# Performance work log

Measured on AMD Instinct MI355X. Metric: run time of the kernel, lower is better.

The kernel has to match this reference:

```python
import jax, jax.numpy as jnp
import numpy as np

N_NODES = 100000
N_EDGES = 1600000
N_GRAPHS = 64
IN_F = 128
H_F = 128
N_CLS = 10


def setup_inputs() -> dict:
    key = jax.random.key(0)
    ks = jax.random.split(key, 10)
    feat = jax.random.normal(ks[0], (N_NODES, IN_F), dtype=jnp.float32)
    W1 = jax.random.normal(ks[1], (IN_F, H_F), dtype=jnp.float32) * 0.05
    b1 = jax.random.normal(ks[2], (H_F,), dtype=jnp.float32) * 0.05
    W2 = jax.random.normal(ks[3], (H_F, H_F), dtype=jnp.float32) * 0.05
    b2 = jax.random.normal(ks[4], (H_F,), dtype=jnp.float32) * 0.05
    Wp = jax.random.normal(ks[5], (H_F, N_CLS), dtype=jnp.float32) * 0.05
    bp = jax.random.normal(ks[6], (N_CLS,), dtype=jnp.float32) * 0.05
    src = jax.random.randint(ks[7], (N_EDGES,), 0, N_NODES, dtype=jnp.int32)
    dst = jax.random.randint(ks[8], (N_EDGES,), 0, N_NODES, dtype=jnp.int32)
    graph_id = jnp.sort(jax.random.randint(ks[9], (N_NODES,), 0, N_GRAPHS, dtype=jnp.int32))
    return {"feat": feat, "W1": W1, "b1": b1, "W2": W2, "b2": b2,
            "Wp": Wp, "bp": bp, "src": src, "dst": dst, "graph_id": graph_id}


def reference(feat, W1, b1, W2, b2, Wp, bp, src, dst, graph_id):
    # copy_u + sum: each dst node sums features of its source neighbors
    def agg(h):
        return jax.ops.segment_sum(h[src], dst, num_segments=N_NODES)

    h = jax.nn.relu(agg(feat) @ W1 + b1)   # conv1 + ReLU
    h = jax.nn.relu(agg(h) @ W2 + b2)      # conv2 + ReLU (num_messagepasses=2)

    # dgl.mean_nodes: per-graph mean pooling over nodes
    sums = jax.ops.segment_sum(h, graph_id, num_segments=N_GRAPHS)      # [G, H]
    cnts = jax.ops.segment_sum(jnp.ones((N_NODES, 1), h.dtype), graph_id,
                               num_segments=N_GRAPHS)                    # [G, 1]
    graph_feats = sums / jnp.maximum(cnts, 1.0)
    return graph_feats @ Wp + bp
```

## Files before the change

### kernel.cpp

```cpp
#include <hip/hip_runtime.h>

#define NF 128
#define NGRAPHS 64
#define NCLS 10
#define NPARTS 256
#define PART_SHIFT 9
#define PART_NODES 512
#define PART_CAP 9216
#define SPLIT_TILE 4096
#define AS_STRIDE 136
#define SRC_BITS 17

typedef __attribute__((ext_vector_type(8))) short bf16x8;
typedef __attribute__((ext_vector_type(4))) float f32x4;
typedef __attribute__((ext_vector_type(8))) unsigned short u16x8;

__device__ __forceinline__ float bf2f(unsigned short u) {
    union { unsigned int i; float f; } v; v.i = ((unsigned int)u) << 16; return v.f;
}
__device__ __forceinline__ unsigned short f2bf(float f) {
    union { float f; unsigned int i; } v; v.f = f;
    unsigned int lsb = (v.i >> 16) & 1;
    v.i += 0x7fffu + lsb;
    return (unsigned short)(v.i >> 16);
}

__device__ __forceinline__ void gather_node(
    const unsigned short* __restrict__ x, const int* __restrict__ offs,
    const int* __restrict__ eid, int node, int n, int c, float acc[8]) {
#pragma unroll
    for (int r = 0; r < 8; ++r) acc[r] = 0.f;
    if (node >= n) return;
    int j = offs[node];
    int end = offs[node + 1];
    for (; j + 8 <= end; j += 8) {
        int s0 = eid[j + 0], s1 = eid[j + 1], s2 = eid[j + 2], s3 = eid[j + 3];
        int s4 = eid[j + 4], s5 = eid[j + 5], s6 = eid[j + 6], s7 = eid[j + 7];
        u16x8 v0 = ((const u16x8*)(x + (size_t)s0 * NF))[c];
        u16x8 v1 = ((const u16x8*)(x + (size_t)s1 * NF))[c];
        u16x8 v2 = ((const u16x8*)(x + (size_t)s2 * NF))[c];
        u16x8 v3 = ((const u16x8*)(x + (size_t)s3 * NF))[c];
        u16x8 v4 = ((const u16x8*)(x + (size_t)s4 * NF))[c];
        u16x8 v5 = ((const u16x8*)(x + (size_t)s5 * NF))[c];
        u16x8 v6 = ((const u16x8*)(x + (size_t)s6 * NF))[c];
        u16x8 v7 = ((const u16x8*)(x + (size_t)s7 * NF))[c];
#pragma unroll
        for (int r = 0; r < 8; ++r)
            acc[r] += ((bf2f(v0[r]) + bf2f(v1[r])) + (bf2f(v2[r]) + bf2f(v3[r])))
                    + ((bf2f(v4[r]) + bf2f(v5[r])) + (bf2f(v6[r]) + bf2f(v7[r])));
    }
    if (j + 4 <= end) {
        int s0 = eid[j + 0], s1 = eid[j + 1], s2 = eid[j + 2], s3 = eid[j + 3];
        u16x8 v0 = ((const u16x8*)(x + (size_t)s0 * NF))[c];
        u16x8 v1 = ((const u16x8*)(x + (size_t)s1 * NF))[c];
        u16x8 v2 = ((const u16x8*)(x + (size_t)s2 * NF))[c];
        u16x8 v3 = ((const u16x8*)(x + (size_t)s3 * NF))[c];
#pragma unroll
        for (int r = 0; r < 8; ++r)
            acc[r] += (bf2f(v0[r]) + bf2f(v1[r])) + (bf2f(v2[r]) + bf2f(v3[r]));
        j += 4;
    }
    for (; j < end; ++j) {
        int s0 = eid[j];
        u16x8 v0 = ((const u16x8*)(x + (size_t)s0 * NF))[c];
#pragma unroll
        for (int r = 0; r < 8; ++r) acc[r] += bf2f(v0[r]);
    }
}

__global__ __launch_bounds__(256) void split_prep_kernel(
    const int* __restrict__ src, const int* __restrict__ dst,
    unsigned int* __restrict__ records, int* __restrict__ gcur,
    const float* __restrict__ feat, unsigned short* __restrict__ featbf,
    const float* __restrict__ W1, const float* __restrict__ W2,
    unsigned short* __restrict__ Wt1, unsigned short* __restrict__ Wt2,
    float* __restrict__ sums, int ne, int nv4) {
    __shared__ unsigned int stage[SPLIT_TILE];
    __shared__ int hcnt[NPARTS];
    __shared__ int hscan[NPARTS];
    __shared__ int hcur[NPARTS];
    __shared__ int hg[NPARTS];
    int t = threadIdx.x;
    int gtid = blockIdx.x * 256 + t;
    int nthreads = gridDim.x * 256;

    for (int i = gtid; i < nv4; i += nthreads) {
        float4 v = ((const float4*)feat)[i];
        ushort4 o;
        o.x = f2bf(v.x); o.y = f2bf(v.y); o.z = f2bf(v.z); o.w = f2bf(v.w);
        ((ushort4*)featbf)[i] = o;
    }
    for (int i = gtid; i < 2 * NF * NF; i += nthreads) {
        const float* W = (i < NF * NF) ? W1 : W2;
        unsigned short* Wt = (i < NF * NF) ? Wt1 : Wt2;
        int id = i & (NF * NF - 1);
        int f = id >> 7;
        int k = id & 127;
        Wt[f * NF + k] = f2bf(W[k * NF + f]);
    }
    for (int i = gtid; i < NGRAPHS * NF; i += nthreads) sums[i] = 0.f;

    int tile0 = blockIdx.x * SPLIT_TILE;
    int cnt = min(SPLIT_TILE, ne - tile0);
    if (cnt <= 0) return;
    hcnt[t] = 0;
    __syncthreads();
    int dv[16], sv[16];
#pragma unroll
    for (int k2 = 0; k2 < 16; ++k2) {
        int i = k2 * 256 + t;
        if (i < cnt) {
            dv[k2] = dst[tile0 + i];
            sv[k2] = src[tile0 + i];
            atomicAdd(&hcnt[dv[k2] >> PART_SHIFT], 1);
        }
    }
    __syncthreads();
    hscan[t] = hcnt[t];
    __syncthreads();
    for (int off = 1; off < NPARTS; off <<= 1) {
        int v = (t >= off) ? hscan[t - off] : 0;
        __syncthreads();
        hscan[t] += v;
        __syncthreads();
    }
    hcur[t] = hscan[t] - hcnt[t];
    hg[t] = hcnt[t] ? atomicAdd(&gcur[t], hcnt[t]) : 0;
    __syncthreads();
#pragma unroll
    for (int k2 = 0; k2 < 16; ++k2) {
        int i = k2 * 256 + t;
        if (i < cnt) {
            int d = dv[k2];
            int pos = atomicAdd(&hcur[d >> PART_SHIFT], 1);
            stage[pos] = (((unsigned int)(d & (PART_NODES - 1))) << SRC_BITS)
                         | (unsigned int)sv[k2];
        }
    }
    __syncthreads();
    int grp = t >> 4;
    int lt = t & 15;
    for (int p = grp; p < NPARTS; p += 16) {
        int c = hcnt[p];
        if (c == 0) continue;
        int b = hscan[p] - c;
        int g = hg[p];
        if (g + c > PART_CAP) c = max(0, PART_CAP - g);
        unsigned int* outp = records + (size_t)p * PART_CAP + g;
        for (int i = lt; i < c; i += 16) outp[i] = stage[b + i];
    }
}

__global__ __launch_bounds__(256) void build_kernel(
    const unsigned int* __restrict__ records, const int* __restrict__ gcur,
    int* __restrict__ offs, int* __restrict__ eid, int n) {
    __shared__ int deg[PART_NODES];
    __shared__ int ps[NPARTS];
    __shared__ int wsum[4];
    __shared__ unsigned int rc[PART_CAP];
    int t = threadIdx.x;
    int p = blockIdx.x;

    ps[t] = min(gcur[t], PART_CAP);
    __syncthreads();
    for (int off = 1; off < NPARTS; off <<= 1) {
        int v = (t >= off) ? ps[t - off] : 0;
        __syncthreads();
        ps[t] += v;
        __syncthreads();
    }
    int L = min(gcur[p], PART_CAP);
    int base_g = ps[p] - L;
    if (p == 0 && t == 0) offs[n] = ps[NPARTS - 1];

    int lo = p << PART_SHIFT;
    int nn = min(n - lo, PART_NODES);
    if (nn <= 0) return;

    deg[t] = 0;
    deg[t + 256] = 0;
    __syncthreads();

    const unsigned int* rp = records + (size_t)p * PART_CAP;
    for (int i = t; i < L; i += 256) {
        unsigned int r = rp[i];
        rc[i] = r;
        atomicAdd(&deg[r >> SRC_BITS], 1);
    }
    __syncthreads();

    int v0 = deg[2 * t];
    int v1 = deg[2 * t + 1];
    int tsum = v0 + v1;
    int lane = t & 63, w = t >> 6;
    int sc = tsum;
    for (int off = 1; off < 64; off <<= 1) {
        int u = __shfl_up(sc, off, 64);
        if (lane >= off) sc += u;
    }
    if (lane == 63) wsum[w] = sc;
    __syncthreads();
    if (t == 0) {
        int a = 0;
        for (int k = 0; k < 4; ++k) { int v = wsum[k]; wsum[k] = a; a += v; }
    }
    __syncthreads();
    int run = sc - tsum + wsum[w];
    deg[2 * t] = run;
    if (2 * t < nn) offs[lo + 2 * t] = base_g + run;
    run += v0;
    deg[2 * t + 1] = run;
    if (2 * t + 1 < nn) offs[lo + 2 * t + 1] = base_g + run;
    __syncthreads();

    for (int i = t; i < L; i += 256) {
        unsigned int r = rc[i];
        int pos = atomicAdd(&deg[r >> SRC_BITS], 1);
        eid[base_g + pos] = (int)(r & ((1u << SRC_BITS) - 1));
    }
}

__global__ __launch_bounds__(256) void gather_gemm1(
    const unsigned short* __restrict__ x, const int* __restrict__ offs,
    const int* __restrict__ eid, const unsigned short* __restrict__ Wt,
    const float* __restrict__ bias, unsigned short* __restrict__ out, int n) {
    __shared__ unsigned short As[16 * AS_STRIDE];
    int wave = threadIdx.x >> 6;
    int lane = threadIdx.x & 63;
    int q = lane >> 4;
    int c = lane & 15;
    int node_base = blockIdx.x * 16;
    int row = wave * 4 + q;

    float acc[8];
    gather_node(x, offs, eid, node_base + row, n, c, acc);
    {
        u16x8 o;
#pragma unroll
        for (int r = 0; r < 8; ++r) o[r] = f2bf(acc[r]);
        *(u16x8*)(&As[row * AS_STRIDE + c * 8]) = o;
    }
    __syncthreads();

    int m16 = c;
    int n0 = wave * 32;
    const unsigned short* b0r = Wt + (size_t)(n0 + m16) * NF + q * 8;
    const unsigned short* b1r = b0r + 16 * NF;
    f32x4 acc0 = {0.f, 0.f, 0.f, 0.f};
    f32x4 acc1 = {0.f, 0.f, 0.f, 0.f};
#pragma unroll
    for (int kk = 0; kk < 4; ++kk) {
        bf16x8 a  = *(const bf16x8*)(&As[m16 * AS_STRIDE + kk * 32 + q * 8]);
        bf16x8 b0 = *(const bf16x8*)(b0r + kk * 32);
        bf16x8 b1 = *(const bf16x8*)(b1r + kk * 32);
        acc0 = __builtin_amdgcn_mfma_f32_16x16x32_bf16(a, b0, acc0, 0, 0, 0);
        acc1 = __builtin_amdgcn_mfma_f32_16x16x32_bf16(a, b1, acc1, 0, 0, 0);
    }
    float bias0 = bias[n0 + m16];
    float bias1 = bias[n0 + 16 + m16];
#pragma unroll
    for (int r = 0; r < 4; ++r) {
        int node = node_base + q * 4 + r;
        if (node >= n) break;
        unsigned short* o = out + (size_t)node * NF;
        o[n0 + m16]      = f2bf(fmaxf(acc0[r] + bias0, 0.f));
        o[n0 + 16 + m16] = f2bf(fmaxf(acc1[r] + bias1, 0.f));
    }
}

__global__ __launch_bounds__(256) void gather_gemm2_pool(
    const unsigned short* __restrict__ x, const int* __restrict__ offs,
    const int* __restrict__ eid, const unsigned short* __restrict__ Wt,
    const float* __restrict__ bias, const int* __restrict__ gid,
    float* __restrict__ sums, int n) {
    __shared__ unsigned short As[16 * AS_STRIDE];
    __shared__ float hblk[16][NF];
    int wave = threadIdx.x >> 6;
    int lane = threadIdx.x & 63;
    int q = lane >> 4;
    int c = lane & 15;
    int node_base = blockIdx.x * 16;
    int row = wave * 4 + q;

    float acc[8];
    gather_node(x, offs, eid, node_base + row, n, c, acc);
    {
        u16x8 o;
#pragma unroll
        for (int r = 0; r < 8; ++r) o[r] = f2bf(acc[r]);
        *(u16x8*)(&As[row * AS_STRIDE + c * 8]) = o;
    }
    __syncthreads();

    int m16 = c;
    int n0 = wave * 32;
    const unsigned short* b0r = Wt + (size_t)(n0 + m16) * NF + q * 8;
    const unsigned short* b1r = b0r + 16 * NF;
    f32x4 acc0 = {0.f, 0.f, 0.f, 0.f};
    f32x4 acc1 = {0.f, 0.f, 0.f, 0.f};
#pragma unroll
    for (int kk = 0; kk < 4; ++kk) {
        bf16x8 a  = *(const bf16x8*)(&As[m16 * AS_STRIDE + kk * 32 + q * 8]);
        bf16x8 b0 = *(const bf16x8*)(b0r + kk * 32);
        bf16x8 b1 = *(const bf16x8*)(b1r + kk * 32);
        acc0 = __builtin_amdgcn_mfma_f32_16x16x32_bf16(a, b0, acc0, 0, 0, 0);
        acc1 = __builtin_amdgcn_mfma_f32_16x16x32_bf16(a, b1, acc1, 0, 0, 0);
    }
    float bias0 = bias[n0 + m16];
    float bias1 = bias[n0 + 16 + m16];
#pragma unroll
    for (int r = 0; r < 4; ++r) {
        int rr = q * 4 + r;
        hblk[rr][n0 + m16]      = fmaxf(acc0[r] + bias0, 0.f);
        hblk[rr][n0 + 16 + m16] = fmaxf(acc1[r] + bias1, 0.f);
    }
    __syncthreads();

    int t = threadIdx.x;
    if (t < NF) {
        float accp = 0.f;
        int cur = -1;
        int lim = min(16, n - node_base);
        for (int i = 0; i < lim; ++i) {
            int g = gid[node_base + i];
            if (g != cur) {
                if (cur >= 0) atomicAdd(&sums[cur * NF + t], accp);
                accp = 0.f;
                cur = g;
            }
            accp += bf2f(f2bf(hblk[i][t]));
        }
        if (cur >= 0) atomicAdd(&sums[cur * NF + t], accp);
    }
}

__device__ __forceinline__ int lower_bound_i(const int* a, int n, int key) {
    int lo = 0, hi = n;
    while (lo < hi) {
        int mid = (lo + hi) >> 1;
        if (a[mid] < key) lo = mid + 1; else hi = mid;
    }
    return lo;
}

__global__ __launch_bounds__(64) void final_kernel(
    const float* __restrict__ sums, const int* __restrict__ gid, int n,
    const float* __restrict__ Wp, const float* __restrict__ bp,
    float* __restrict__ out) {
    __shared__ int range[2];
    int g = blockIdx.x;
    int c = threadIdx.x;
    if (c == 0) range[0] = lower_bound_i(gid, n, g);
    if (c == 1) range[1] = lower_bound_i(gid, n, g + 1);
    __syncthreads();
    if (c >= NCLS) return;
    float cnt = fmaxf((float)(range[1] - range[0]), 1.0f);
    float inv = 1.0f / cnt;
    float acc = bp[c];
#pragma unroll 8
    for (int k = 0; k < NF; ++k) {
        acc += sums[g * NF + k] * inv * Wp[k * NCLS + c];
    }
    out[g * NCLS + c] = acc;
}

extern "C" void kernel_launch(void* const* d_in, const int* in_sizes, int n_in,
                              void* d_out, int out_size, void* d_ws, size_t ws_size,
                              hipStream_t stream) {
    const float* feat = (const float*)d_in[0];
    const float* W1   = (const float*)d_in[1];
    const float* b1   = (const float*)d_in[2];
    const float* W2   = (const float*)d_in[3];
    const float* b2   = (const float*)d_in[4];
    const float* Wp   = (const float*)d_in[5];
    const float* bp   = (const float*)d_in[6];
    const int*   src  = (const int*)d_in[7];
    const int*   dst  = (const int*)d_in[8];
    const int*   gid  = (const int*)d_in[9];

    int ne = in_sizes[7];
    int n  = in_sizes[9];

    unsigned short* featbf = (unsigned short*)d_ws;
    unsigned short* h1     = featbf + (size_t)n * NF;
    unsigned int* records = (unsigned int*)(h1 + (size_t)n * NF);
    int* eid      = (int*)(records + (size_t)NPARTS * PART_CAP);
    float* sums   = (float*)(eid + ne);
    int* gcur     = (int*)(sums + NGRAPHS * NF);
    unsigned short* Wt1 = (unsigned short*)(gcur + NPARTS);
    unsigned short* Wt2 = Wt1 + NF * NF;
    int* offs     = (int*)(Wt2 + NF * NF);

    int nv4 = n * NF / 4;
    int splitblocks = (ne + SPLIT_TILE - 1) / SPLIT_TILE;
    int buildblocks = (n + PART_NODES - 1) >> PART_SHIFT;
    int ggblocks = (n + 15) / 16;

    hipMemsetAsync(gcur, 0, NPARTS * sizeof(int), stream);
    split_prep_kernel<<<splitblocks, 256, 0, stream>>>(
        src, dst, records, gcur, feat, featbf, W1, W2, Wt1, Wt2, sums, ne, nv4);
    build_kernel<<<buildblocks, 256, 0, stream>>>(records, gcur, offs, eid, n);

    gather_gemm1<<<ggblocks, 256, 0, stream>>>(featbf, offs, eid, Wt1, b1, h1, n);
    gather_gemm2_pool<<<ggblocks, 256, 0, stream>>>(h1, offs, eid, Wt2, b2, gid, sums, n);
    final_kernel<<<NGRAPHS, 64, 0, stream>>>(sums, gid, n, Wp, bp, (float*)d_out);
}
```

Before: 306.8 us.

## Fuse CSR construction into gather-GEMM kernels using per-block local LDS CSR

```diff
diff --git a/kernel.cpp b/kernel.cpp
--- a/kernel.cpp
+++ b/kernel.cpp
@@ -10,6 +10,7 @@
 #define SPLIT_TILE 4096
 #define AS_STRIDE 136
 #define SRC_BITS 17
+#define QCAP 2560
 
 typedef __attribute__((ext_vector_type(8))) short bf16x8;
 typedef __attribute__((ext_vector_type(4))) float f32x4;
@@ -25,17 +26,15 @@
     return (unsigned short)(v.i >> 16);
 }
 
-__device__ __forceinline__ void gather_node(
-    const unsigned short* __restrict__ x, const int* __restrict__ offs,
-    const int* __restrict__ eid, int node, int n, int c, float acc[8]) {
+__device__ __forceinline__ void gather_node_l(
+    const unsigned short* __restrict__ x, const int* eid_l,
+    int beg, int end, int c, float acc[8]) {
 #pragma unroll
     for (int r = 0; r < 8; ++r) acc[r] = 0.f;
-    if (node >= n) return;
-    int j = offs[node];
-    int end = offs[node + 1];
+    int j = beg;
     for (; j + 8 <= end; j += 8) {
-        int s0 = eid[j + 0], s1 = eid[j + 1], s2 = eid[j + 2], s3 = eid[j + 3];
-        int s4 = eid[j + 4], s5 = eid[j + 5], s6 = eid[j + 6], s7 = eid[j + 7];
+        int s0 = eid_l[j + 0], s1 = eid_l[j + 1], s2 = eid_l[j + 2], s3 = eid_l[j + 3];
+        int s4 = eid_l[j + 4], s5 = eid_l[j + 5], s6 = eid_l[j + 6], s7 = eid_l[j + 7];
         u16x8 v0 = ((const u16x8*)(x + (size_t)s0 * NF))[c];
         u16x8 v1 = ((const u16x8*)(x + (size_t)s1 * NF))[c];
         u16x8 v2 = ((const u16x8*)(x + (size_t)s2 * NF))[c];
@@ -50,7 +49,7 @@
                     + ((bf2f(v4[r]) + bf2f(v5[r])) + (bf2f(v6[r]) + bf2f(v7[r])));
     }
     if (j + 4 <= end) {
-        int s0 = eid[j + 0], s1 = eid[j + 1], s2 = eid[j + 2], s3 = eid[j + 3];
+        int s0 = eid_l[j + 0], s1 = eid_l[j + 1], s2 = eid_l[j + 2], s3 = eid_l[j + 3];
         u16x8 v0 = ((const u16x8*)(x + (size_t)s0 * NF))[c];
         u16x8 v1 = ((const u16x8*)(x + (size_t)s1 * NF))[c];
         u16x8 v2 = ((const u16x8*)(x + (size_t)s2 * NF))[c];
@@ -61,11 +60,53 @@
         j += 4;
     }
     for (; j < end; ++j) {
-        int s0 = eid[j];
+        int s0 = eid_l[j];
         u16x8 v0 = ((const u16x8*)(x + (size_t)s0 * NF))[c];
 #pragma unroll
         for (int r = 0; r < 8; ++r) acc[r] += bf2f(v0[r]);
     }
+}
+
+__device__ __forceinline__ void build_local_csr(
+    const unsigned int* __restrict__ records, const int* __restrict__ gcur,
+    int p, int quad, unsigned int* tmp, int* eid_l,
+    int* deg, int* incl, int* cursor, int* nmatch_s) {
+    int t = threadIdx.x;
+    if (t < 128) deg[t] = 0;
+    if (t == 0) *nmatch_s = 0;
+    __syncthreads();
+    int L = min(gcur[p], PART_CAP);
+    const unsigned int* rp = records + (size_t)p * PART_CAP;
+    for (int i = t; i < L; i += 256) {
+        unsigned int r = rp[i];
+        int d = (int)(r >> SRC_BITS);
+        if ((d >> 7) == quad) {
+            int pos = atomicAdd(nmatch_s, 1);
+            if (pos < QCAP) {
+                tmp[pos] = r;
+                atomicAdd(&deg[d & 127], 1);
+            }
+        }
+    }
+    __syncthreads();
+    int nm = min(*nmatch_s, QCAP);
+    if (t < 128) incl[t] = deg[t];
+    __syncthreads();
+    for (int off = 1; off < 128; off <<= 1) {
+        int v = (t < 128 && t >= off) ? incl[t - off] : 0;
+        __syncthreads();
+        if (t < 128) incl[t] += v;
+        __syncthreads();
+    }
+    if (t < 128) cursor[t] = incl[t] - deg[t];
+    __syncthreads();
+    for (int i = t; i < nm; i += 256) {
+        unsigned int r = tmp[i];
+        int d = (int)((r >> SRC_BITS) & 127);
+        int pos = atomicAdd(&cursor[d], 1);
+        eid_l[pos] = (int)(r & ((1u << SRC_BITS) - 1));
+    }
+    __syncthreads();
 }
 
 __global__ __launch_bounds__(256) void split_prep_kernel(
@@ -151,187 +192,159 @@
     }
 }
 
-__global__ __launch_bounds__(256) void build_kernel(
-    const unsigned int* __restrict__ records, const int* __restrict__ gcur,
-    int* __restrict__ offs, int* __restrict__ eid, int n) {
-    __shared__ int deg[PART_NODES];
-    __shared__ int ps[NPARTS];
-    __shared__ int wsum[4];
-    __shared__ unsigned int rc[PART_CAP];
+__global__ __launch_bounds__(256) void gather_gemm1(
+    const unsigned short* __restrict__ x, const unsigned int* __restrict__ records,
+    const int* __restrict__ gcur, const unsigned short* __restrict__ Wt,
+    const float* __restrict__ bias, unsigned short* __restrict__ out, int n) {
+    __shared__ unsigned int tmp[QCAP];
+    __shared__ int eid_l[QCAP];
+    __shared__ int deg[128], incl[128], cursor[128];
+    __shared__ int nmatch_s;
+    __shared__ unsigned short As[16 * AS_STRIDE];
     int t = threadIdx.x;
-    int p = blockIdx.x;
-
-    ps[t] = min(gcur[t], PART_CAP);
-    __syncthreads();
-    for (int off = 1; off < NPARTS; off <<= 1) {
-        int v = (t >= off) ? ps[t - off] : 0;
-        __syncthreads();
-        ps[t] += v;
-        __syncthreads();
-    }
-    int L = min(gcur[p], PART_CAP);
-    int base_g = ps[p] - L;
-    if (p == 0 && t == 0) offs[n] = ps[NPARTS - 1];
-
-    int lo = p << PART_SHIFT;
-    int nn = min(n - lo, PART_NODES);
-    if (nn <= 0) return;
-
-    deg[t] = 0;
-    deg[t + 256] = 0;
-    __syncthreads();
-
-    const unsigned int* rp = records + (size_t)p * PART_CAP;
-    for (int i = t; i < L; i += 256) {
-        unsigned int r = rp[i];
-        rc[i] = r;
-        atomicAdd(&deg[r >> SRC_BITS], 1);
-    }
-    __syncthreads();
-
-    int v0 = deg[2 * t];
-    int v1 = deg[2 * t + 1];
-    int tsum = v0 + v1;
-    int lane = t & 63, w = t >> 6;
-    int sc = tsum;
-    for (int off = 1; off < 64; off <<= 1) {
-        int u = __shfl_up(sc, off, 64);
-        if (lane >= off) sc += u;
-    }
-    if (lane == 63) wsum[w] = sc;
-    __syncthreads();
-    if (t == 0) {
-        int a = 0;
-        for (int k = 0; k < 4; ++k) { int v = wsum[k]; wsum[k] = a; a += v; }
-    }
-    __syncthreads();
-    int run = sc - tsum + wsum[w];
-    deg[2 * t] = run;
-    if (2 * t < nn) offs[lo + 2 * t] = base_g + run;
-    run += v0;
-    deg[2 * t + 1] = run;
-    if (2 * t + 1 < nn) offs[lo + 2 * t + 1] = base_g + run;
-    __syncthreads();
-
-    for (int i = t; i < L; i += 256) {
-        unsigned int r = rc[i];
-        int pos = atomicAdd(&deg[r >> SRC_BITS], 1);
-        eid[base_g + pos] = (int)(r & ((1u << SRC_BITS) - 1));
-    }
-}
-
-__global__ __launch_bounds__(256) void gather_gemm1(
-    const unsigned short* __restrict__ x, const int* __restrict__ offs,
-    const int* __restrict__ eid, const unsigned short* __restrict__ Wt,
-    const float* __restrict__ bias, unsigned short* __restrict__ out, int n) {
-    __shared__ unsigned short As[16 * AS_STRIDE];
-    int wave = threadIdx.x >> 6;
-    int lane = threadIdx.x & 63;
+    int p = blockIdx.x >> 2;
+    int quad = blockIdx.x & 3;
+    int node_lo = (p << PART_SHIFT) + (quad << 7);
+
+    build_local_csr(records, gcur, p, quad, tmp, eid_l, deg, incl, cursor, &nmatch_s);
+
+    int wave = t >> 6;
+    int lane = t & 63;
     int q = lane >> 4;
     int c = lane & 15;
-    int node_base = blockIdx.x * 16;
     int row = wave * 4 + q;
-
-    float acc[8];
-    gather_node(x, offs, eid, node_base + row, n, c, acc);
-    {
-        u16x8 o;
-#pragma unroll
-        for (int r = 0; r < 8; ++r) o[r] = f2bf(acc[r]);
-        *(u16x8*)(&As[row * AS_STRIDE + c * 8]) = o;
-    }
-    __syncthreads();
-
     int m16 = c;
     int n0 = wave * 32;
     const unsigned short* b0r = Wt + (size_t)(n0 + m16) * NF + q * 8;
     const unsigned short* b1r = b0r + 16 * NF;
-    f32x4 acc0 = {0.f, 0.f, 0.f, 0.f};
-    f32x4 acc1 = {0.f, 0.f, 0.f, 0.f};
-#pragma unroll
-    for (int kk = 0; kk < 4; ++kk) {
-        bf16x8 a  = *(const bf16x8*)(&As[m16 * AS_STRIDE + kk * 32 + q * 8]);
-        bf16x8 b0 = *(const bf16x8*)(b0r + kk * 32);
-        bf16x8 b1 = *(const bf16x8*)(b1r + kk * 32);
-        acc0 = __builtin_amdgcn_mfma_f32_16x16x32_bf16(a, b0, acc0, 0, 0, 0);
-        acc1 = __builtin_amdgcn_mfma_f32_16x16x32_bf16(a, b1, acc1, 0, 0, 0);
-    }
     float bias0 = bias[n0 + m16];
     float bias1 = bias[n0 + 16 + m16];
-#pragma unroll
-    for (int r = 0; r < 4; ++r) {
-        int node = node_base + q * 4 + r;
-        if (node >= n) break;
-        unsigned short* o = out + (size_t)node * NF;
-        o[n0 + m16]      = f2bf(fmaxf(acc0[r] + bias0, 0.f));
-        o[n0 + 16 + m16] = f2bf(fmaxf(acc1[r] + bias1, 0.f));
+
+    for (int tile = 0; tile < 8; ++tile) {
+        int dl = tile * 16 + row;
+        int node = node_lo + dl;
+        float acc[8];
+        if (node < n) {
+            gather_node_l(x, eid_l, incl[dl] - deg[dl], incl[dl], c, acc);
+        } else {
+#pragma unroll
+            for (int r = 0; r < 8; ++r) acc[r] = 0.f;
+        }
+        {
+            u16x8 o;
+#pragma unroll
+            for (int r = 0; r < 8; ++r) o[r] = f2bf(acc[r]);
+            *(u16x8*)(&As[row * AS_STRIDE + c * 8]) = o;
+        }
+        __syncthreads();
+
+        f32x4 acc0 = {0.f, 0.f, 0.f, 0.f};
+        f32x4 acc1 = {0.f, 0.f, 0.f, 0.f};
+#pragma unroll
+        for (int kk = 0; kk < 4; ++kk) {
+            bf16x8 a  = *(const bf16x8*)(&As[m16 * AS_STRIDE + kk * 32 + q * 8]);
+            bf16x8 b0 = *(const bf16x8*)(b0r + kk * 32);
+            bf16x8 b1 = *(const bf16x8*)(b1r + kk * 32);
+            acc0 = __builtin_amdgcn_mfma_f32_16x16x32_bf16(a, b0, acc0, 0, 0, 0);
+            acc1 = __builtin_amdgcn_mfma_f32_16x16x32_bf16(a, b1, acc1, 0, 0, 0);
+        }
+#pragma unroll
+        for (int r = 0; r < 4; ++r) {
+            int node2 = node_lo + tile * 16 + q * 4 + r;
+            if (node2 >= n) break;
+            unsigned short* o = out + (size_t)node2 * NF;
+            o[n0 + m16]      = f2bf(fmaxf(acc0[r] + bias0, 0.f));
+            o[n0 + 16 + m16] = f2bf(fmaxf(acc1[r] + bias1, 0.f));
+        }
+        __syncthreads();
     }
 }
 
 __global__ __launch_bounds__(256) void gather_gemm2_pool(
-    const unsigned short* __restrict__ x, const int* __restrict__ offs,
-    const int* __restrict__ eid, const unsigned short* __restrict__ Wt,
+    const unsigned short* __restrict__ x, const unsigned int* __restrict__ records,
+    const int* __restrict__ gcur, const unsigned short* __restrict__ Wt,
     const float* __restrict__ bias, const int* __restrict__ gid,
     float* __restrict__ sums, int n) {
+    __shared__ unsigned int tmp[QCAP];
+    __shared__ int eid_l[QCAP];
+    __shared__ int deg[128], incl[128], cursor[128];
+    __shared__ int nmatch_s;
     __shared__ unsigned short As[16 * AS_STRIDE];
     __shared__ float hblk[16][NF];
-    int wave = threadIdx.x >> 6;
-    int lane = threadIdx.x & 63;
+    int t = threadIdx.x;
+    int p = blockIdx.x >> 2;
+    int quad = blockIdx.x & 3;
+    int node_lo = (p << PART_SHIFT) + (quad << 7);
+
+    build_local_csr(records, gcur, p, quad, tmp, eid_l, deg, incl, cursor, &nmatch_s);
+
+    int wave = t >> 6;
+    int lane = t & 63;
     int q = lane >> 4;
     int c = lane & 15;
-    int node_base = blockIdx.x * 16;
     int row = wave * 4 + q;
-
-    float acc[8];
-    gather_node(x, offs, eid, node_base + row, n, c, acc);
-    {
-        u16x8 o;
-#pragma unroll
-        for (int r = 0; r < 8; ++r) o[r] = f2bf(acc[r]);
-        *(u16x8*)(&As[row * AS_STRIDE + c * 8]) = o;
-    }
-    __syncthreads();
-
     int m16 = c;
     int n0 = wave * 32;
     const unsigned short* b0r = Wt + (size_t)(n0 + m16) * NF + q * 8;
     const unsigned short* b1r = b0r + 16 * NF;
-    f32x4 acc0 = {0.f, 0.f, 0.f, 0.f};
-    f32x4 acc1 = {0.f, 0.f, 0.f, 0.f};
-#pragma unroll
-    for (int kk = 0; kk < 4; ++kk) {
-        bf16x8 a  = *(const bf16x8*)(&As[m16 * AS_STRIDE + kk * 32 + q * 8]);
-        bf16x8 b0 = *(const bf16x8*)(b0r + kk * 32);
-        bf16x8 b1 = *(const bf16x8*)(b1r + kk * 32);
-        acc0 = __builtin_amdgcn_mfma_f32_16x16x32_bf16(a, b0, acc0, 0, 0, 0);
-        acc1 = __builtin_amdgcn_mfma_f32_16x16x32_bf16(a, b1, acc1, 0, 0, 0);
-    }
     float bias0 = bias[n0 + m16];
     float bias1 = bias[n0 + 16 + m16];
-#pragma unroll
-    for (int r = 0; r < 4; ++r) {
-        int rr = q * 4 + r;
-        hblk[rr][n0 + m16]      = fmaxf(acc0[r] + bias0, 0.f);
-        hblk[rr][n0 + 16 + m16] = fmaxf(acc1[r] + bias1, 0.f);
-    }
-    __syncthreads();
-
-    int t = threadIdx.x;
-    if (t < NF) {
-        float accp = 0.f;
-        int cur = -1;
-        int lim = min(16, n - node_base);
-        for (int i = 0; i < lim; ++i) {
-            int g = gid[node_base + i];
-            if (g != cur) {
-                if (cur >= 0) atomicAdd(&sums[cur * NF + t], accp);
-                accp = 0.f;
-                cur = g;
+
+    float accp = 0.f;
+    int curg = -1;
+
+    for (int tile = 0; tile < 8; ++tile) {
+        int dl = tile * 16 + row;
+        int node = node_lo + dl;
+        float acc[8];
+        if (node < n) {
+            gather_node_l(x, eid_l, incl[dl] - deg[dl], incl[dl], c, acc);
+        } else {
+#pragma unroll
+            for (int r = 0; r < 8; ++r) acc[r] = 0.f;
+        }
+        {
+            u16x8 o;
+#pragma unroll
+            for (int r = 0; r < 8; ++r) o[r] = f2bf(acc[r]);
+            *(u16x8*)(&As[row * AS_STRIDE + c * 8]) = o;
+        }
+        __syncthreads();
+
+        f32x4 acc0 = {0.f, 0.f, 0.f, 0.f};
+        f32x4 acc1 = {0.f, 0.f, 0.f, 0.f};
+#pragma unroll
+        for (int kk = 0; kk < 4; ++kk) {
+            bf16x8 a  = *(const bf16x8*)(&As[m16 * AS_STRIDE + kk * 32 + q * 8]);
+            bf16x8 b0 = *(const bf16x8*)(b0r + kk * 32);
+            bf16x8 b1 = *(const bf16x8*)(b1r + kk * 32);
+            acc0 = __builtin_amdgcn_mfma_f32_16x16x32_bf16(a, b0, acc0, 0, 0, 0);
+            acc1 = __builtin_amdgcn_mfma_f32_16x16x32_bf16(a, b1, acc1, 0, 0, 0);
+        }
+#pragma unroll
+        for (int r = 0; r < 4; ++r) {
+            int rr = q * 4 + r;
+            hblk[rr][n0 + m16]      = fmaxf(acc0[r] + bias0, 0.f);
+            hblk[rr][n0 + 16 + m16] = fmaxf(acc1[r] + bias1, 0.f);
+        }
+        __syncthreads();
+
+        if (t < NF) {
+            int node_base = node_lo + tile * 16;
+            int lim = min(16, n - node_base);
+            for (int i = 0; i < lim; ++i) {
+                int g = gid[node_base + i];
+                if (g != curg) {
+                    if (curg >= 0) atomicAdd(&sums[curg * NF + t], accp);
+                    accp = 0.f;
+                    curg = g;
+                }
+                accp += bf2f(f2bf(hblk[i][t]));
             }
-            accp += bf2f(f2bf(hblk[i][t]));
-        }
-        if (cur >= 0) atomicAdd(&sums[cur * NF + t], accp);
-    }
+        }
+        __syncthreads();
+    }
+    if (t < NF && curg >= 0) atomicAdd(&sums[curg * NF + t], accp);
 }
 
 __device__ __forceinline__ int lower_bound_i(const int* a, int n, int key) {
@@ -349,19 +362,21 @@
     float* __restrict__ out) {
     __shared__ int range[2];
     int g = blockIdx.x;
-    int c = threadIdx.x;
-    if (c == 0) range[0] = lower_bound_i(gid, n, g);
-    if (c == 1) range[1] = lower_bound_i(gid, n, g + 1);
-    __syncthreads();
-    if (c >= NCLS) return;
+    int lane = threadIdx.x;
+    if (lane == 0) range[0] = lower_bound_i(gid, n, g);
+    if (lane == 1) range[1] = lower_bound_i(gid, n, g + 1);
+    __syncthreads();
     float cnt = fmaxf((float)(range[1] - range[0]), 1.0f);
     float inv = 1.0f / cnt;
-    float acc = bp[c];
-#pragma unroll 8
-    for (int k = 0; k < NF; ++k) {
-        acc += sums[g * NF + k] * inv * Wp[k * NCLS + c];
-    }
-    out[g * NCLS + c] = acc;
+    float s0 = sums[g * NF + lane] * inv;
+    float s1 = sums[g * NF + 64 + lane] * inv;
+#pragma unroll
+    for (int c = 0; c < NCLS; ++c) {
+        float p = s0 * Wp[lane * NCLS + c] + s1 * Wp[(64 + lane) * NCLS + c];
+#pragma unroll
+        for (int m = 1; m < 64; m <<= 1) p += __shfl_xor(p, m, 64);
+        if (lane == 0) out[g * NCLS + c] = p + bp[c];
+    }
 }
 
 extern "C" void kernel_launch(void* const* d_in, const int* in_sizes, int n_in,
@@ -384,24 +399,21 @@
     unsigned short* featbf = (unsigned short*)d_ws;
     unsigned short* h1     = featbf + (size_t)n * NF;
     unsigned int* records = (unsigned int*)(h1 + (size_t)n * NF);
-    int* eid      = (int*)(records + (size_t)NPARTS * PART_CAP);
-    float* sums   = (float*)(eid + ne);
+    float* sums   = (float*)(records + (size_t)NPARTS * PART_CAP);
     int* gcur     = (int*)(sums + NGRAPHS * NF);
     unsigned short* Wt1 = (unsigned short*)(gcur + NPARTS);
     unsigned short* Wt2 = Wt1 + NF * NF;
-    int* offs     = (int*)(Wt2 + NF * NF);
 
     int nv4 = n * NF / 4;
     int splitblocks = (ne + SPLIT_TILE - 1) / SPLIT_TILE;
-    int buildblocks = (n + PART_NODES - 1) >> PART_SHIFT;
-    int ggblocks = (n + 15) / 16;
+    int nparts = (n + PART_NODES - 1) >> PART_SHIFT;
+    int ggblocks = nparts * 4;
 
     hipMemsetAsync(gcur, 0, NPARTS * sizeof(int), stream);
     split_prep_kernel<<<splitblocks, 256, 0, stream>>>(
         src, dst, records, gcur, feat, featbf, W1, W2, Wt1, Wt2, sums, ne, nv4);
-    build_kernel<<<buildblocks, 256, 0, stream>>>(records, gcur, offs, eid, n);
-
-    gather_gemm1<<<ggblocks, 256, 0, stream>>>(featbf, offs, eid, Wt1, b1, h1, n);
-    gather_gemm2_pool<<<ggblocks, 256, 0, stream>>>(h1, offs, eid, Wt2, b2, gid, sums, n);
+
+    gather_gemm1<<<ggblocks, 256, 0, stream>>>(featbf, records, gcur, Wt1, b1, h1, n);
+    gather_gemm2_pool<<<ggblocks, 256, 0, stream>>>(h1, records, gcur, Wt2, b2, gid, sums, n);
     final_kernel<<<NGRAPHS, 64, 0, stream>>>(sums, gid, n, Wp, bp, (float*)d_out);
 }
```

Result: slower. 378.1 us (+23.2%).

## Privatize LDS histograms per wave and fuse final projection into last gemm2 block

Applied to the files above, without the earlier changes.

```diff
diff --git a/kernel.cpp b/kernel.cpp
--- a/kernel.cpp
+++ b/kernel.cpp
@@ -76,9 +76,9 @@
     unsigned short* __restrict__ Wt1, unsigned short* __restrict__ Wt2,
     float* __restrict__ sums, int ne, int nv4) {
     __shared__ unsigned int stage[SPLIT_TILE];
+    __shared__ int hcnt_w[4][NPARTS];
     __shared__ int hcnt[NPARTS];
     __shared__ int hscan[NPARTS];
-    __shared__ int hcur[NPARTS];
     __shared__ int hg[NPARTS];
     int t = threadIdx.x;
     int gtid = blockIdx.x * 256 + t;
@@ -103,8 +103,9 @@
     int tile0 = blockIdx.x * SPLIT_TILE;
     int cnt = min(SPLIT_TILE, ne - tile0);
     if (cnt <= 0) return;
-    hcnt[t] = 0;
-    __syncthreads();
+    hcnt_w[0][t] = 0; hcnt_w[1][t] = 0; hcnt_w[2][t] = 0; hcnt_w[3][t] = 0;
+    __syncthreads();
+    int wv = t >> 6;
     int dv[16], sv[16];
 #pragma unroll
     for (int k2 = 0; k2 < 16; ++k2) {
@@ -112,10 +113,12 @@
         if (i < cnt) {
             dv[k2] = dst[tile0 + i];
             sv[k2] = src[tile0 + i];
-            atomicAdd(&hcnt[dv[k2] >> PART_SHIFT], 1);
+            atomicAdd(&hcnt_w[wv][dv[k2] >> PART_SHIFT], 1);
         }
     }
     __syncthreads();
+    int c0 = hcnt_w[0][t], c1 = hcnt_w[1][t], c2 = hcnt_w[2][t], c3 = hcnt_w[3][t];
+    hcnt[t] = c0 + c1 + c2 + c3;
     hscan[t] = hcnt[t];
     __syncthreads();
     for (int off = 1; off < NPARTS; off <<= 1) {
@@ -124,7 +127,11 @@
         hscan[t] += v;
         __syncthreads();
     }
-    hcur[t] = hscan[t] - hcnt[t];
+    int excl = hscan[t] - hcnt[t];
+    hcnt_w[0][t] = excl;
+    hcnt_w[1][t] = excl + c0;
+    hcnt_w[2][t] = excl + c0 + c1;
+    hcnt_w[3][t] = excl + c0 + c1 + c2;
     hg[t] = hcnt[t] ? atomicAdd(&gcur[t], hcnt[t]) : 0;
     __syncthreads();
 #pragma unroll
@@ -132,7 +139,7 @@
         int i = k2 * 256 + t;
         if (i < cnt) {
             int d = dv[k2];
-            int pos = atomicAdd(&hcur[d >> PART_SHIFT], 1);
+            int pos = atomicAdd(&hcnt_w[wv][d >> PART_SHIFT], 1);
             stage[pos] = (((unsigned int)(d & (PART_NODES - 1))) << SRC_BITS)
                          | (unsigned int)sv[k2];
         }
@@ -154,7 +161,7 @@
 __global__ __launch_bounds__(256) void build_kernel(
     const unsigned int* __restrict__ records, const int* __restrict__ gcur,
     int* __restrict__ offs, int* __restrict__ eid, int n) {
-    __shared__ int deg[PART_NODES];
+    __shared__ int deg_w[4][PART_NODES];
     __shared__ int ps[NPARTS];
     __shared__ int wsum[4];
     __shared__ unsigned int rc[PART_CAP];
@@ -177,20 +184,25 @@
     int nn = min(n - lo, PART_NODES);
     if (nn <= 0) return;
 
-    deg[t] = 0;
-    deg[t + 256] = 0;
-    __syncthreads();
-
+#pragma unroll
+    for (int w2 = 0; w2 < 4; ++w2) { deg_w[w2][t] = 0; deg_w[w2][t + 256] = 0; }
+    __syncthreads();
+
+    int wv = t >> 6;
     const unsigned int* rp = records + (size_t)p * PART_CAP;
     for (int i = t; i < L; i += 256) {
         unsigned int r = rp[i];
         rc[i] = r;
-        atomicAdd(&deg[r >> SRC_BITS], 1);
-    }
-    __syncthreads();
-
-    int v0 = deg[2 * t];
-    int v1 = deg[2 * t + 1];
+        atomicAdd(&deg_w[wv][r >> SRC_BITS], 1);
+    }
+    __syncthreads();
+
+    int a0 = deg_w[0][2 * t],     a1 = deg_w[1][2 * t];
+    int a2 = deg_w[2][2 * t],     a3 = deg_w[3][2 * t];
+    int b0 = deg_w[0][2 * t + 1], b1 = deg_w[1][2 * t + 1];
+    int b2 = deg_w[2][2 * t + 1], b3 = deg_w[3][2 * t + 1];
+    int v0 = a0 + a1 + a2 + a3;
+    int v1 = b0 + b1 + b2 + b3;
     int tsum = v0 + v1;
     int lane = t & 63, w = t >> 6;
     int sc = tsum;
@@ -206,16 +218,22 @@
     }
     __syncthreads();
     int run = sc - tsum + wsum[w];
-    deg[2 * t] = run;
+    deg_w[0][2 * t] = run;
+    deg_w[1][2 * t] = run + a0;
+    deg_w[2][2 * t] = run + a0 + a1;
+    deg_w[3][2 * t] = run + a0 + a1 + a2;
     if (2 * t < nn) offs[lo + 2 * t] = base_g + run;
     run += v0;
-    deg[2 * t + 1] = run;
+    deg_w[0][2 * t + 1] = run;
+    deg_w[1][2 * t + 1] = run + b0;
+    deg_w[2][2 * t + 1] = run + b0 + b1;
+    deg_w[3][2 * t + 1] = run + b0 + b1 + b2;
     if (2 * t + 1 < nn) offs[lo + 2 * t + 1] = base_g + run;
     __syncthreads();
 
     for (int i = t; i < L; i += 256) {
         unsigned int r = rc[i];
-        int pos = atomicAdd(&deg[r >> SRC_BITS], 1);
+        int pos = atomicAdd(&deg_w[wv][r >> SRC_BITS], 1);
         eid[base_g + pos] = (int)(r & ((1u << SRC_BITS) - 1));
     }
 }
@@ -268,13 +286,26 @@
     }
 }
 
-__global__ __launch_bounds__(256) void gather_gemm2_pool(
+__device__ __forceinline__ int lower_bound_i(const int* a, int n, int key) {
+    int lo = 0, hi = n;
+    while (lo < hi) {
+        int mid = (lo + hi) >> 1;
+        if (a[mid] < key) lo = mid + 1; else hi = mid;
+    }
+    return lo;
+}
+
+__global__ __launch_bounds__(256) void gather_gemm2_pool_final(
     const unsigned short* __restrict__ x, const int* __restrict__ offs,
     const int* __restrict__ eid, const unsigned short* __restrict__ Wt,
     const float* __restrict__ bias, const int* __restrict__ gid,
-    float* __restrict__ sums, int n) {
+    float* __restrict__ sums, int* __restrict__ done_cnt,
+    const float* __restrict__ Wp, const float* __restrict__ bp,
+    float* __restrict__ out, int n) {
     __shared__ unsigned short As[16 * AS_STRIDE];
     __shared__ float hblk[16][NF];
+    __shared__ int bnd[NGRAPHS + 1];
+    __shared__ int is_last;
     int wave = threadIdx.x >> 6;
     int lane = threadIdx.x & 63;
     int q = lane >> 4;
@@ -332,36 +363,33 @@
         }
         if (cur >= 0) atomicAdd(&sums[cur * NF + t], accp);
     }
-}
-
-__device__ __forceinline__ int lower_bound_i(const int* a, int n, int key) {
-    int lo = 0, hi = n;
-    while (lo < hi) {
-        int mid = (lo + hi) >> 1;
-        if (a[mid] < key) lo = mid + 1; else hi = mid;
-    }
-    return lo;
-}
-
-__global__ __launch_bounds__(64) void final_kernel(
-    const float* __restrict__ sums, const int* __restrict__ gid, int n,
-    const float* __restrict__ Wp, const float* __restrict__ bp,
-    float* __restrict__ out) {
-    __shared__ int range[2];
-    int g = blockIdx.x;
-    int c = threadIdx.x;
-    if (c == 0) range[0] = lower_bound_i(gid, n, g);
-    if (c == 1) range[1] = lower_bound_i(gid, n, g + 1);
-    __syncthreads();
-    if (c >= NCLS) return;
-    float cnt = fmaxf((float)(range[1] - range[0]), 1.0f);
-    float inv = 1.0f / cnt;
-    float acc = bp[c];
-#pragma unroll 8
-    for (int k = 0; k < NF; ++k) {
-        acc += sums[g * NF + k] * inv * Wp[k * NCLS + c];
-    }
-    out[g * NCLS + c] = acc;
+
+    __syncthreads();
+    if (t == 0) {
+        int prev = __hip_atomic_fetch_add(done_cnt, 1, __ATOMIC_ACQ_REL,
+                                          __HIP_MEMORY_SCOPE_AGENT);
+        is_last = (prev == (int)gridDim.x - 1);
+    }
+    __syncthreads();
+    if (!is_last) return;
+
+    if (t <= NGRAPHS) bnd[t] = lower_bound_i(gid, n, t);
+    __syncthreads();
+    for (int g = wave; g < NGRAPHS; g += 4) {
+        float cntf = fmaxf((float)(bnd[g + 1] - bnd[g]), 1.0f);
+        float inv = 1.0f / cntf;
+        float s0 = __hip_atomic_load(&sums[g * NF + lane], __ATOMIC_RELAXED,
+                                     __HIP_MEMORY_SCOPE_AGENT) * inv;
+        float s1 = __hip_atomic_load(&sums[g * NF + 64 + lane], __ATOMIC_RELAXED,
+                                     __HIP_MEMORY_SCOPE_AGENT) * inv;
+#pragma unroll
+        for (int cc = 0; cc < NCLS; ++cc) {
+            float pv = s0 * Wp[lane * NCLS + cc] + s1 * Wp[(64 + lane) * NCLS + cc];
+#pragma unroll
+            for (int m = 1; m < 64; m <<= 1) pv += __shfl_xor(pv, m, 64);
+            if (lane == 0) out[g * NCLS + cc] = pv + bp[cc];
+        }
+    }
 }
 
 extern "C" void kernel_launch(void* const* d_in, const int* in_sizes, int n_in,
@@ -387,7 +415,8 @@
     int* eid      = (int*)(records + (size_t)NPARTS * PART_CAP);
     float* sums   = (float*)(eid + ne);
     int* gcur     = (int*)(sums + NGRAPHS * NF);
-    unsigned short* Wt1 = (unsigned short*)(gcur + NPARTS);
+    int* done_cnt = gcur + NPARTS;
+    unsigned short* Wt1 = (unsigned short*)(gcur + NPARTS + 4);
     unsigned short* Wt2 = Wt1 + NF * NF;
     int* offs     = (int*)(Wt2 + NF * NF);
 
@@ -396,12 +425,12 @@
     int buildblocks = (n + PART_NODES - 1) >> PART_SHIFT;
     int ggblocks = (n + 15) / 16;
 
-    hipMemsetAsync(gcur, 0, NPARTS * sizeof(int), stream);
+    hipMemsetAsync(gcur, 0, (NPARTS + 1) * sizeof(int), stream);
     split_prep_kernel<<<splitblocks, 256, 0, stream>>>(
         src, dst, records, gcur, feat, featbf, W1, W2, Wt1, Wt2, sums, ne, nv4);
     build_kernel<<<buildblocks, 256, 0, stream>>>(records, gcur, offs, eid, n);
 
     gather_gemm1<<<ggblocks, 256, 0, stream>>>(featbf, offs, eid, Wt1, b1, h1, n);
-    gather_gemm2_pool<<<ggblocks, 256, 0, stream>>>(h1, offs, eid, Wt2, b2, gid, sums, n);
-    final_kernel<<<NGRAPHS, 64, 0, stream>>>(sums, gid, n, Wp, bp, (float*)d_out);
-}
+    gather_gemm2_pool_final<<<ggblocks, 256, 0, stream>>>(
+        h1, offs, eid, Wt2, b2, gid, sums, done_cnt, Wp, bp, (float*)d_out, n);
+}
```

After: 490.9 us. 1.6x slower.
